# Kernel optimization log

Measured on AMD Instinct MI355X. Metric: run time of the kernel, lower is better.

The kernel has to match this reference:

```python
import jax, jax.numpy as jnp
import numpy as np

B, S, D, H = 2, 4096, 1024, 16
HD = D // H  # 64
BASE = 10000.0


def setup_inputs() -> dict:
    key = jax.random.key(0)
    ks = jax.random.split(key, 11)
    s = 1.0 / np.sqrt(D)
    return {
        "consulta": jax.random.normal(ks[0], (B, S, D), jnp.float32),
        "chave": jax.random.normal(ks[1], (B, S, D), jnp.float32),
        "valor": jax.random.normal(ks[2], (B, S, D), jnp.float32),
        "Wq": jax.random.normal(ks[3], (D, D), jnp.float32) * s,
        "bq": jnp.zeros((D,), jnp.float32),
        "Wk": jax.random.normal(ks[4], (D, D), jnp.float32) * s,
        "bk": jnp.zeros((D,), jnp.float32),
        "Wv": jax.random.normal(ks[5], (D, D), jnp.float32) * s,
        "bv": jnp.zeros((D,), jnp.float32),
        "Wo": jax.random.normal(ks[6], (D, D), jnp.float32) * s,
        "bo": jnp.zeros((D,), jnp.float32),
    }


def _rope(x):
    # x: [B, H, S, HD]; rotate interleaved (even, odd) pairs
    seq = x.shape[2]
    theta = 1.0 / (BASE ** (jnp.arange(0, HD, 2, dtype=jnp.float32) / HD))  # [HD/2]
    angles = jnp.arange(seq, dtype=jnp.float32)[:, None] * theta[None, :]  # [S, HD/2]
    cos, sin = jnp.cos(angles), jnp.sin(angles)
    xr = x.reshape(*x.shape[:-1], HD // 2, 2)
    x_re, x_im = xr[..., 0], xr[..., 1]
    out_re = x_re * cos - x_im * sin
    out_im = x_re * sin + x_im * cos
    return jnp.stack([out_re, out_im], axis=-1).reshape(x.shape)


def reference(consulta, chave, valor, Wq, bq, Wk, bk, Wv, bv, Wo, bo):
    b, s, _ = consulta.shape
    # projections (torch Linear: x @ W.T + b)
    Q = consulta @ Wq.T + bq
    K = chave @ Wk.T + bk
    V = valor @ Wv.T + bv
    # [B, H, S, HD]
    Q = Q.reshape(b, s, H, HD).transpose(0, 2, 1, 3)
    K = K.reshape(b, s, H, HD).transpose(0, 2, 1, 3)
    V = V.reshape(b, s, H, HD).transpose(0, 2, 1, 3)
    Q = _rope(Q)
    K = _rope(K)
    scores = jnp.einsum('bhqd,bhkd->bhqk', Q, K) / jnp.sqrt(jnp.float32(HD))
    weights = jax.nn.softmax(scores, axis=-1)  # dropout p=0 -> identity
    out = jnp.einsum('bhqk,bhkd->bhqd', weights, V)
    out = out.transpose(0, 2, 1, 3).reshape(b, s, D)
    return out @ Wo.T + bo
```

## Files before the change

### kernel.cpp

```cpp
#include <hip/hip_runtime.h>
#include <hip/hip_bf16.h>

typedef __attribute__((ext_vector_type(8))) short short8;
typedef __attribute__((ext_vector_type(4))) float f32x4;
typedef __attribute__((ext_vector_type(4))) unsigned short ushort4v;
typedef __attribute__((ext_vector_type(4))) float float4v;
typedef __attribute__((ext_vector_type(2))) unsigned int uint32x2;

#define NB 2
#define NS 4096
#define ND 1024
#define NH 16
#define NHD 64

#define QSCALE 0.18033688011112042f

__device__ __forceinline__ unsigned short f2bf(float x) {
    union { float f; unsigned u; } v; v.f = x;
    unsigned r = v.u + 0x7FFFu + ((v.u >> 16) & 1u);
    return (unsigned short)(r >> 16);
}

__device__ __forceinline__ unsigned cvt_pk_bf16(float lo, float hi) {
    unsigned r;
    asm("v_cvt_pk_bf16_f32 %0, %1, %2" : "=v"(r) : "v"(lo), "v"(hi));
    return r;
}

__device__ __forceinline__ void gload_lds16(const unsigned short* g, unsigned short* l) {
    __builtin_amdgcn_global_load_lds(
        (const __attribute__((address_space(1))) void*)g,
        (__attribute__((address_space(3))) void*)l,
        16, 0, 0);
}

__global__ void rope_table_kernel(float* __restrict__ cosT, float* __restrict__ sinT) {
    int i = blockIdx.x * blockDim.x + threadIdx.x;
    int p = i & 31, s = i >> 5;
    float theta = exp2f(-(float)(2 * p) * (13.287712379549449f / 64.0f));
    float ang = (float)s * theta;
    float sv, cv;
    sincosf(ang, &sv, &cv);
    cosT[i] = cv; sinT[i] = sv;
}

__global__ void cast_bf16_kernel(const float* __restrict__ in, unsigned short* __restrict__ out, int n8) {
    int i = blockIdx.x * blockDim.x + threadIdx.x;
    if (i >= n8) return;
    float4v a0 = *(const float4v*)(&in[(size_t)i * 8]);
    float4v a1 = *(const float4v*)(&in[(size_t)i * 8 + 4]);
    short8 s8;
    s8[0] = (short)f2bf(a0.x); s8[1] = (short)f2bf(a0.y);
    s8[2] = (short)f2bf(a0.z); s8[3] = (short)f2bf(a0.w);
    s8[4] = (short)f2bf(a1.x); s8[5] = (short)f2bf(a1.y);
    s8[6] = (short)f2bf(a1.z); s8[7] = (short)f2bf(a1.w);
    *(short8*)(&out[(size_t)i * 8]) = s8;
}

template<int EPI>
__global__ __launch_bounds__(256, 2) void gemm_kernel(
    const unsigned short* __restrict__ A,
    const unsigned short* __restrict__ Wb,
    const float* __restrict__ bias,
    void* __restrict__ outv,
    const float* __restrict__ cosT,
    const float* __restrict__ sinT,
    float oscale)
{
    __shared__ unsigned short As[128 * 32];
    __shared__ unsigned short Bs[128 * 32];
    const int t = threadIdx.x;
    const int wave = t >> 6, lane = t & 63;
    const int quad = lane >> 4, l15 = lane & 15;
    const int wm = (wave & 1) * 64, wn = (wave >> 1) * 64;
    const int m0 = blockIdx.y * 128, n0 = blockIdx.x * 128;

    f32x4 acc[4][4];
#pragma unroll
    for (int i = 0; i < 4; i++)
#pragma unroll
        for (int j = 0; j < 4; j++)
            acc[i][j] = f32x4{0.f, 0.f, 0.f, 0.f};

    for (int k0 = 0; k0 < ND; k0 += 32) {
#pragma unroll
        for (int p = 0; p < 2; p++) {
            int idx = p * 256 + t;
            int r = idx >> 2, c = (idx & 3) * 8;
            unsigned short* ldsA = &As[(size_t)(p * 256 + wave * 64) * 8];
            unsigned short* ldsB = &Bs[(size_t)(p * 256 + wave * 64) * 8];
            gload_lds16(&A[(size_t)(m0 + r) * ND + k0 + c], ldsA);
            gload_lds16(&Wb[(size_t)(n0 + r) * ND + k0 + c], ldsB);
        }
        __syncthreads();

        short8 af[4], bfr[4];
#pragma unroll
        for (int mt = 0; mt < 4; mt++)
            af[mt] = *(const short8*)(&As[(wm + mt * 16 + l15) * 32 + quad * 8]);
#pragma unroll
        for (int nt = 0; nt < 4; nt++)
            bfr[nt] = *(const short8*)(&Bs[(wn + nt * 16 + l15) * 32 + quad * 8]);
#pragma unroll
        for (int mt = 0; mt < 4; mt++)
#pragma unroll
            for (int nt = 0; nt < 4; nt++) {
                if (EPI == 0)
                    acc[mt][nt] = __builtin_amdgcn_mfma_f32_16x16x32_bf16(bfr[nt], af[mt], acc[mt][nt], 0, 0, 0);
                else
                    acc[mt][nt] = __builtin_amdgcn_mfma_f32_16x16x32_bf16(af[mt], bfr[nt], acc[mt][nt], 0, 0, 0);
            }
        __syncthreads();
    }

    if (EPI == 0) {
        float* out = (float*)outv;
#pragma unroll
        for (int mt = 0; mt < 4; mt++) {
            int gm = m0 + wm + mt * 16 + l15;
#pragma unroll
            for (int nt = 0; nt < 4; nt++) {
                int gn0 = n0 + wn + nt * 16 + quad * 4;
                float4v fv;
#pragma unroll
                for (int r = 0; r < 4; r++)
                    fv[r] = acc[mt][nt][r] + bias[gn0 + r];
                *(float4v*)(&out[(size_t)gm * ND + gn0]) = fv;
            }
        }
    } else if (EPI == 1) {
        unsigned short* out = (unsigned short*)outv;
#pragma unroll
        for (int nt = 0; nt < 4; nt++) {
            int gn = n0 + wn + nt * 16 + l15;
            int h = gn >> 6, hd = gn & 63, pr = hd >> 1, im = gn & 1;
            float bv = bias[gn];
#pragma unroll
            for (int mt = 0; mt < 4; mt++) {
                int gm0 = m0 + wm + mt * 16 + quad * 4;
#pragma unroll
                for (int r = 0; r < 4; r++) {
                    int gm = gm0 + r;
                    int b = gm >> 12, s = gm & 4095;
                    float v = acc[mt][nt][r] + bv;
                    float pv = __shfl_xor(v, 1, 64);
                    float cv = cosT[s * 32 + pr], sv = sinT[s * 32 + pr];
                    float o = im ? (pv * sv + v * cv) : (v * cv - pv * sv);
                    out[((size_t)(b * NH + h) * NS + s) * NHD + hd] = f2bf(o * oscale);
                }
            }
        }
    } else {
        unsigned short* out = (unsigned short*)outv;
#pragma unroll
        for (int nt = 0; nt < 4; nt++) {
            int gn = n0 + wn + nt * 16 + l15;
            int h = gn >> 6, hd = gn & 63;
            float bv = bias[gn];
#pragma unroll
            for (int mt = 0; mt < 4; mt++) {
                int gm0 = m0 + wm + mt * 16 + quad * 4;
                int b = gm0 >> 12, s0 = gm0 & 4095;
                ushort4v pk;
#pragma unroll
                for (int r = 0; r < 4; r++)
                    pk[r] = f2bf(acc[mt][nt][r] + bv);
                *(ushort4v*)(&out[((size_t)(b * NH + h) * NHD + hd) * NS + s0]) = pk;
            }
        }
    }
}

__global__ __launch_bounds__(256, 2) void flash_kernel(
    const unsigned short* __restrict__ Qr,
    const unsigned short* __restrict__ Kr,
    const unsigned short* __restrict__ Vt,
    unsigned short* __restrict__ Yatt)
{
    __shared__ unsigned short Ks[128 * 72];
    __shared__ unsigned short Vs[64 * 136];
    __shared__ unsigned short Pw[4][16 * 136];
    const int t = threadIdx.x;
    const int wave = t >> 6, lane = t & 63;
    const int quad = lane >> 4, l15 = lane & 15;
    const int bh = blockIdx.y;
    const int qb = blockIdx.x * 128;
    const int wq = wave * 32;
    const size_t base = (size_t)bh * NS * NHD;

    short8 qf[2][2];
#pragma unroll
    for (int nt = 0; nt < 2; nt++)
#pragma unroll
        for (int kk = 0; kk < 2; kk++)
            qf[nt][kk] = *(const short8*)(&Qr[base + (size_t)(qb + wq + nt * 16 + l15) * NHD + kk * 32 + quad * 8]);

    f32x4 accO[4][2];
#pragma unroll
    for (int i = 0; i < 4; i++)
#pragma unroll
        for (int j = 0; j < 2; j++)
            accO[i][j] = f32x4{0.f, 0.f, 0.f, 0.f};
    float mrow[2] = {-1e30f, -1e30f};
    float lrow[2] = {0.f, 0.f};

    for (int j0 = 0; j0 < NS; j0 += 128) {
#pragma unroll
        for (int p = 0; p < 4; p++) {
            int idx = p * 256 + t;
            { int r = idx >> 3, c = (idx & 7) * 8;
              *(short8*)(&Ks[r * 72 + c]) = *(const short8*)(&Kr[base + (size_t)(j0 + r) * NHD + c]); }
            { int r = idx >> 4, c = (idx & 15) * 8;
              *(short8*)(&Vs[r * 136 + c]) = *(const short8*)(&Vt[(size_t)(bh * NHD + r) * NS + j0 + c]); }
        }
        __syncthreads();

        f32x4 sa[8][2];
#pragma unroll
        for (int mt = 0; mt < 8; mt++)
#pragma unroll
            for (int nt = 0; nt < 2; nt++)
                sa[mt][nt] = f32x4{0.f, 0.f, 0.f, 0.f};
#pragma unroll
        for (int kk = 0; kk < 2; kk++)
#pragma unroll
            for (int mt = 0; mt < 8; mt++) {
                short8 ak = *(const short8*)(&Ks[(mt * 16 + l15) * 72 + kk * 32 + quad * 8]);
#pragma unroll
                for (int nt = 0; nt < 2; nt++)
                    sa[mt][nt] = __builtin_amdgcn_mfma_f32_16x16x32_bf16(ak, qf[nt][kk], sa[mt][nt], 0, 0, 0);
            }

#pragma unroll
        for (int nt = 0; nt < 2; nt++) {
            float mm[8];
#pragma unroll
            for (int mt = 0; mt < 8; mt++)
                mm[mt] = fmaxf(fmaxf(sa[mt][nt][0], sa[mt][nt][1]),
                               fmaxf(sa[mt][nt][2], sa[mt][nt][3]));
            float mx = fmaxf(fmaxf(fmaxf(mm[0], mm[1]), fmaxf(mm[2], mm[3])),
                             fmaxf(fmaxf(mm[4], mm[5]), fmaxf(mm[6], mm[7])));
            mx = fmaxf(mx, __shfl_xor(mx, 16, 64));
            mx = fmaxf(mx, __shfl_xor(mx, 32, 64));
            float mnew = fmaxf(mrow[nt], mx);
            float alpha = exp2f(mrow[nt] - mnew);
            float ls0 = 0.f, ls1 = 0.f, ls2 = 0.f, ls3 = 0.f;
#pragma unroll
            for (int mt = 0; mt < 8; mt++) {
                float p0 = exp2f(sa[mt][nt][0] - mnew);
                float p1 = exp2f(sa[mt][nt][1] - mnew);
                float p2 = exp2f(sa[mt][nt][2] - mnew);
                float p3 = exp2f(sa[mt][nt][3] - mnew);
                ls0 += p0; ls1 += p1; ls2 += p2; ls3 += p3;
                uint32x2 pk;
                pk.x = cvt_pk_bf16(p0, p1);
                pk.y = cvt_pk_bf16(p2, p3);
                *(uint32x2*)(&Pw[wave][l15 * 136 + mt * 16 + quad * 4]) = pk;
            }
            float lsum = (ls0 + ls1) + (ls2 + ls3);
            lsum += __shfl_xor(lsum, 16, 64);
            lsum += __shfl_xor(lsum, 32, 64);
            lrow[nt] = lrow[nt] * alpha + lsum;
            mrow[nt] = mnew;
#pragma unroll
            for (int mt2 = 0; mt2 < 4; mt2++)
#pragma unroll
                for (int r = 0; r < 4; r++)
                    accO[mt2][nt][r] *= alpha;

#pragma unroll
            for (int kk2 = 0; kk2 < 4; kk2++) {
                short8 av[4];
#pragma unroll
                for (int mt2 = 0; mt2 < 4; mt2++)
                    av[mt2] = *(const short8*)(&Vs[(mt2 * 16 + l15) * 136 + kk2 * 32 + quad * 8]);
                short8 bp = *(const short8*)(&Pw[wave][l15 * 136 + kk2 * 32 + quad * 8]);
#pragma unroll
                for (int mt2 = 0; mt2 < 4; mt2++)
                    accO[mt2][nt] = __builtin_amdgcn_mfma_f32_16x16x32_bf16(av[mt2], bp, accO[mt2][nt], 0, 0, 0);
            }
        }
        __syncthreads();
    }

    int b = bh >> 4, h = bh & 15;
#pragma unroll
    for (int nt = 0; nt < 2; nt++) {
        float rl = 1.f / lrow[nt];
        int s = qb + wq + nt * 16 + l15;
#pragma unroll
        for (int mt2 = 0; mt2 < 4; mt2++) {
            uint32x2 pk;
            pk.x = cvt_pk_bf16(accO[mt2][nt][0] * rl, accO[mt2][nt][1] * rl);
            pk.y = cvt_pk_bf16(accO[mt2][nt][2] * rl, accO[mt2][nt][3] * rl);
            *(uint32x2*)(&Yatt[((size_t)(b * NS + s)) * ND + h * NHD + mt2 * 16 + quad * 4]) = pk;
        }
    }
}

extern "C" void kernel_launch(void* const* d_in, const int* in_sizes, int n_in,
                              void* d_out, int out_size, void* d_ws, size_t ws_size,
                              hipStream_t stream) {
    const float* consulta = (const float*)d_in[0];
    const float* chave    = (const float*)d_in[1];
    const float* valor    = (const float*)d_in[2];
    const float* Wq = (const float*)d_in[3];
    const float* bq = (const float*)d_in[4];
    const float* Wk = (const float*)d_in[5];
    const float* bk = (const float*)d_in[6];
    const float* Wv = (const float*)d_in[7];
    const float* bv = (const float*)d_in[8];
    const float* Wo = (const float*)d_in[9];
    const float* bo = (const float*)d_in[10];

    const size_t NX = (size_t)8192 * 1024;

    float* cosT = (float*)d_ws;
    float* sinT = cosT + (size_t)NS * 32;
    unsigned short* Qrb = (unsigned short*)(sinT + (size_t)NS * 32);
    unsigned short* Krb = Qrb + NX;
    unsigned short* Vtb = Krb + NX;
    unsigned short* Yat = Vtb + NX;
    unsigned short* Abf = Yat + NX;
    unsigned short* Wbf = Abf + NX;

    rope_table_kernel<<<NS * 32 / 256, 256, 0, stream>>>(cosT, sinT);

    const int ACT8 = (int)(NX / 8);
    const int W8 = ND * ND / 8;

    dim3 ggrid(8, 64);

    cast_bf16_kernel<<<ACT8 / 256, 256, 0, stream>>>(consulta, Abf, ACT8);
    cast_bf16_kernel<<<W8 / 256, 256, 0, stream>>>(Wq, Wbf, W8);
    gemm_kernel<1><<<ggrid, 256, 0, stream>>>(Abf, Wbf, bq, Qrb, cosT, sinT, QSCALE);

    cast_bf16_kernel<<<ACT8 / 256, 256, 0, stream>>>(chave, Abf, ACT8);
    cast_bf16_kernel<<<W8 / 256, 256, 0, stream>>>(Wk, Wbf, W8);
    gemm_kernel<1><<<ggrid, 256, 0, stream>>>(Abf, Wbf, bk, Krb, cosT, sinT, 1.0f);

    cast_bf16_kernel<<<ACT8 / 256, 256, 0, stream>>>(valor, Abf, ACT8);
    cast_bf16_kernel<<<W8 / 256, 256, 0, stream>>>(Wv, Wbf, W8);
    gemm_kernel<2><<<ggrid, 256, 0, stream>>>(Abf, Wbf, bv, Vtb, cosT, sinT, 1.0f);

    flash_kernel<<<dim3(32, 32), 256, 0, stream>>>(Qrb, Krb, Vtb, Yat);

    cast_bf16_kernel<<<W8 / 256, 256, 0, stream>>>(Wo, Wbf, W8);
    gemm_kernel<0><<<ggrid, 256, 0, stream>>>(Yat, Wbf, bo, d_out, cosT, sinT, 1.0f);
}
```

Before: 587.6 us.

## Prefetch next K/V tile into registers and batch PV MFMAs with lazy rescale

Loads the next K/V tile from global memory into registers before the current tile's compute, then writes it to shared memory after a barrier, so global latency overlaps the MFMA work. The P tile now stores both 16-row groups, which lets the PV MFMAs for both row groups be interleaved in one loop. The online-softmax rescale is skipped while the running max grows by at most 8 (log2 units). s_setprio is raised around the MFMA blocks. The cost is more registers from the prefetch buffers and more LDS for Pw, which may reduce occupancy under launch_bounds(256,2).

```diff
diff --git a/kernel.cpp b/kernel.cpp
--- a/kernel.cpp
+++ b/kernel.cpp
@@ -179,7 +179,7 @@
 {
     __shared__ unsigned short Ks[128 * 72];
     __shared__ unsigned short Vs[64 * 136];
-    __shared__ unsigned short Pw[4][16 * 136];
+    __shared__ unsigned short Pw[4][32 * 136];
     const int t = threadIdx.x;
     const int wave = t >> 6, lane = t & 63;
     const int quad = lane >> 4, l15 = lane & 15;
@@ -204,16 +204,35 @@
     float mrow[2] = {-1e30f, -1e30f};
     float lrow[2] = {0.f, 0.f};
 
+#pragma unroll
+    for (int p = 0; p < 4; p++) {
+        int idx = p * 256 + t;
+        { int r = idx >> 3, c = (idx & 7) * 8;
+          *(short8*)(&Ks[r * 72 + c]) = *(const short8*)(&Kr[base + (size_t)r * NHD + c]); }
+        { int r = idx >> 4, c = (idx & 15) * 8;
+          *(short8*)(&Vs[r * 136 + c]) = *(const short8*)(&Vt[(size_t)(bh * NHD + r) * NS + c]); }
+    }
+    __syncthreads();
+
     for (int j0 = 0; j0 < NS; j0 += 128) {
-#pragma unroll
-        for (int p = 0; p < 4; p++) {
-            int idx = p * 256 + t;
-            { int r = idx >> 3, c = (idx & 7) * 8;
-              *(short8*)(&Ks[r * 72 + c]) = *(const short8*)(&Kr[base + (size_t)(j0 + r) * NHD + c]); }
-            { int r = idx >> 4, c = (idx & 15) * 8;
-              *(short8*)(&Vs[r * 136 + c]) = *(const short8*)(&Vt[(size_t)(bh * NHD + r) * NS + j0 + c]); }
-        }
-        __syncthreads();
+        const bool more = (j0 + 128) < NS;
+
+        short8 kpr0, kpr1, kpr2, kpr3, vpr0, vpr1, vpr2, vpr3;
+        if (more) {
+            int j1 = j0 + 128;
+#pragma unroll
+            for (int p = 0; p < 4; p++) {
+                int idx = p * 256 + t;
+                int rk = idx >> 3, ck = (idx & 7) * 8;
+                int rv = idx >> 4, cv = (idx & 15) * 8;
+                short8 kv = *(const short8*)(&Kr[base + (size_t)(j1 + rk) * NHD + ck]);
+                short8 vv = *(const short8*)(&Vt[(size_t)(bh * NHD + rv) * NS + j1 + cv]);
+                if (p == 0) { kpr0 = kv; vpr0 = vv; }
+                else if (p == 1) { kpr1 = kv; vpr1 = vv; }
+                else if (p == 2) { kpr2 = kv; vpr2 = vv; }
+                else { kpr3 = kv; vpr3 = vv; }
+            }
+        }
 
         f32x4 sa[8][2];
 #pragma unroll
@@ -221,6 +240,7 @@
 #pragma unroll
             for (int nt = 0; nt < 2; nt++)
                 sa[mt][nt] = f32x4{0.f, 0.f, 0.f, 0.f};
+        __builtin_amdgcn_s_setprio(1);
 #pragma unroll
         for (int kk = 0; kk < 2; kk++)
 #pragma unroll
@@ -230,6 +250,7 @@
                 for (int nt = 0; nt < 2; nt++)
                     sa[mt][nt] = __builtin_amdgcn_mfma_f32_16x16x32_bf16(ak, qf[nt][kk], sa[mt][nt], 0, 0, 0);
             }
+        __builtin_amdgcn_s_setprio(0);
 
 #pragma unroll
         for (int nt = 0; nt < 2; nt++) {
@@ -242,42 +263,66 @@
                              fmaxf(fmaxf(mm[4], mm[5]), fmaxf(mm[6], mm[7])));
             mx = fmaxf(mx, __shfl_xor(mx, 16, 64));
             mx = fmaxf(mx, __shfl_xor(mx, 32, 64));
-            float mnew = fmaxf(mrow[nt], mx);
-            float alpha = exp2f(mrow[nt] - mnew);
+            if (!__all(mx <= mrow[nt] + 8.0f)) {
+                float mnew = fmaxf(mrow[nt], mx);
+                float alpha = exp2f(mrow[nt] - mnew);
+                lrow[nt] *= alpha;
+#pragma unroll
+                for (int mt2 = 0; mt2 < 4; mt2++)
+#pragma unroll
+                    for (int r = 0; r < 4; r++)
+                        accO[mt2][nt][r] *= alpha;
+                mrow[nt] = mnew;
+            }
+            float mcur = mrow[nt];
             float ls0 = 0.f, ls1 = 0.f, ls2 = 0.f, ls3 = 0.f;
 #pragma unroll
             for (int mt = 0; mt < 8; mt++) {
-                float p0 = exp2f(sa[mt][nt][0] - mnew);
-                float p1 = exp2f(sa[mt][nt][1] - mnew);
-                float p2 = exp2f(sa[mt][nt][2] - mnew);
-                float p3 = exp2f(sa[mt][nt][3] - mnew);
+                float p0 = exp2f(sa[mt][nt][0] - mcur);
+                float p1 = exp2f(sa[mt][nt][1] - mcur);
+                float p2 = exp2f(sa[mt][nt][2] - mcur);
+                float p3 = exp2f(sa[mt][nt][3] - mcur);
                 ls0 += p0; ls1 += p1; ls2 += p2; ls3 += p3;
                 uint32x2 pk;
                 pk.x = cvt_pk_bf16(p0, p1);
                 pk.y = cvt_pk_bf16(p2, p3);
-                *(uint32x2*)(&Pw[wave][l15 * 136 + mt * 16 + quad * 4]) = pk;
+                *(uint32x2*)(&Pw[wave][(nt * 16 + l15) * 136 + mt * 16 + quad * 4]) = pk;
             }
             float lsum = (ls0 + ls1) + (ls2 + ls3);
             lsum += __shfl_xor(lsum, 16, 64);
             lsum += __shfl_xor(lsum, 32, 64);
-            lrow[nt] = lrow[nt] * alpha + lsum;
-            mrow[nt] = mnew;
+            lrow[nt] += lsum;
+        }
+
+        __builtin_amdgcn_s_setprio(1);
+#pragma unroll
+        for (int kk2 = 0; kk2 < 4; kk2++) {
+            short8 av[4], bp[2];
 #pragma unroll
             for (int mt2 = 0; mt2 < 4; mt2++)
-#pragma unroll
-                for (int r = 0; r < 4; r++)
-                    accO[mt2][nt][r] *= alpha;
-
-#pragma unroll
-            for (int kk2 = 0; kk2 < 4; kk2++) {
-                short8 av[4];
-#pragma unroll
-                for (int mt2 = 0; mt2 < 4; mt2++)
-                    av[mt2] = *(const short8*)(&Vs[(mt2 * 16 + l15) * 136 + kk2 * 32 + quad * 8]);
-                short8 bp = *(const short8*)(&Pw[wave][l15 * 136 + kk2 * 32 + quad * 8]);
-#pragma unroll
-                for (int mt2 = 0; mt2 < 4; mt2++)
-                    accO[mt2][nt] = __builtin_amdgcn_mfma_f32_16x16x32_bf16(av[mt2], bp, accO[mt2][nt], 0, 0, 0);
+                av[mt2] = *(const short8*)(&Vs[(mt2 * 16 + l15) * 136 + kk2 * 32 + quad * 8]);
+#pragma unroll
+            for (int nt = 0; nt < 2; nt++)
+                bp[nt] = *(const short8*)(&Pw[wave][(nt * 16 + l15) * 136 + kk2 * 32 + quad * 8]);
+#pragma unroll
+            for (int mt2 = 0; mt2 < 4; mt2++)
+#pragma unroll
+                for (int nt = 0; nt < 2; nt++)
+                    accO[mt2][nt] = __builtin_amdgcn_mfma_f32_16x16x32_bf16(av[mt2], bp[nt], accO[mt2][nt], 0, 0, 0);
+        }
+        __builtin_amdgcn_s_setprio(0);
+
+        __syncthreads();
+        if (more) {
+#pragma unroll
+            for (int p = 0; p < 4; p++) {
+                int idx = p * 256 + t;
+                int rk = idx >> 3, ck = (idx & 7) * 8;
+                int rv = idx >> 4, cv = (idx & 15) * 8;
+                short8 kv = (p == 0) ? kpr0 : (p == 1) ? kpr1 : (p == 2) ? kpr2 : kpr3;
+                short8 vv = (p == 0) ? vpr0 : (p == 1) ? vpr1 : (p == 2) ? vpr2 : vpr3;
+                *(short8*)(&Ks[rk * 72 + ck]) = kv;
+                *(short8*)(&Vs[rv * 136 + cv]) = vv;
             }
         }
         __syncthreads();
```

Result: faster. 560.1 us (-4.7%).

## Rewrite flash attention inner loop with 32x32 MFMA and register-resident P

Applied to the files above, without the earlier changes.

Switches the flash kernel from 16x16x32 to 32x32x16 bf16 MFMA tiles so each wave owns 32 query rows with one running max and sum per lane. The softmax probabilities stay in registers and are rearranged with v_permlane32_swap instead of going through a per-wave LDS buffer, which removes LDS traffic and the shared P array. It also skips the accumulator rescale unless the row max grows by more than 8 (lazy rescaling), and raises wave priority around the MFMA blocks. The larger 16-float accumulators increase register pressure, which may hurt occupancy under launch_bounds(256,2).

```diff
diff --git a/kernel.cpp b/kernel.cpp
--- a/kernel.cpp
+++ b/kernel.cpp
@@ -3,9 +3,11 @@
 
 typedef __attribute__((ext_vector_type(8))) short short8;
 typedef __attribute__((ext_vector_type(4))) float f32x4;
+typedef __attribute__((ext_vector_type(16))) float f32x16;
 typedef __attribute__((ext_vector_type(4))) unsigned short ushort4v;
 typedef __attribute__((ext_vector_type(4))) float float4v;
 typedef __attribute__((ext_vector_type(2))) unsigned int uint32x2;
+typedef __attribute__((ext_vector_type(4))) unsigned int uint32x4;
 
 #define NB 2
 #define NS 4096
@@ -179,30 +181,26 @@
 {
     __shared__ unsigned short Ks[128 * 72];
     __shared__ unsigned short Vs[64 * 136];
-    __shared__ unsigned short Pw[4][16 * 136];
     const int t = threadIdx.x;
     const int wave = t >> 6, lane = t & 63;
-    const int quad = lane >> 4, l15 = lane & 15;
+    const int l31 = lane & 31, h = lane >> 5;
     const int bh = blockIdx.y;
     const int qb = blockIdx.x * 128;
     const int wq = wave * 32;
     const size_t base = (size_t)bh * NS * NHD;
 
-    short8 qf[2][2];
-#pragma unroll
-    for (int nt = 0; nt < 2; nt++)
-#pragma unroll
-        for (int kk = 0; kk < 2; kk++)
-            qf[nt][kk] = *(const short8*)(&Qr[base + (size_t)(qb + wq + nt * 16 + l15) * NHD + kk * 32 + quad * 8]);
-
-    f32x4 accO[4][2];
-#pragma unroll
-    for (int i = 0; i < 4; i++)
-#pragma unroll
-        for (int j = 0; j < 2; j++)
-            accO[i][j] = f32x4{0.f, 0.f, 0.f, 0.f};
-    float mrow[2] = {-1e30f, -1e30f};
-    float lrow[2] = {0.f, 0.f};
+    short8 qf[4];
+#pragma unroll
+    for (int ks = 0; ks < 4; ks++)
+        qf[ks] = *(const short8*)(&Qr[base + (size_t)(qb + wq + l31) * NHD + ks * 16 + h * 8]);
+
+    f32x16 accO[2];
+#pragma unroll
+    for (int dt = 0; dt < 2; dt++)
+#pragma unroll
+        for (int r = 0; r < 16; r++)
+            accO[dt][r] = 0.f;
+    float mrow = -1e30f, lrow = 0.f;
 
     for (int j0 = 0; j0 < NS; j0 += 128) {
 #pragma unroll
@@ -215,87 +213,101 @@
         }
         __syncthreads();
 
-        f32x4 sa[8][2];
-#pragma unroll
-        for (int mt = 0; mt < 8; mt++)
-#pragma unroll
-            for (int nt = 0; nt < 2; nt++)
-                sa[mt][nt] = f32x4{0.f, 0.f, 0.f, 0.f};
-#pragma unroll
-        for (int kk = 0; kk < 2; kk++)
-#pragma unroll
-            for (int mt = 0; mt < 8; mt++) {
-                short8 ak = *(const short8*)(&Ks[(mt * 16 + l15) * 72 + kk * 32 + quad * 8]);
-#pragma unroll
-                for (int nt = 0; nt < 2; nt++)
-                    sa[mt][nt] = __builtin_amdgcn_mfma_f32_16x16x32_bf16(ak, qf[nt][kk], sa[mt][nt], 0, 0, 0);
-            }
-
-#pragma unroll
-        for (int nt = 0; nt < 2; nt++) {
-            float mm[8];
-#pragma unroll
-            for (int mt = 0; mt < 8; mt++)
-                mm[mt] = fmaxf(fmaxf(sa[mt][nt][0], sa[mt][nt][1]),
-                               fmaxf(sa[mt][nt][2], sa[mt][nt][3]));
-            float mx = fmaxf(fmaxf(fmaxf(mm[0], mm[1]), fmaxf(mm[2], mm[3])),
-                             fmaxf(fmaxf(mm[4], mm[5]), fmaxf(mm[6], mm[7])));
-            mx = fmaxf(mx, __shfl_xor(mx, 16, 64));
-            mx = fmaxf(mx, __shfl_xor(mx, 32, 64));
-            float mnew = fmaxf(mrow[nt], mx);
-            float alpha = exp2f(mrow[nt] - mnew);
-            float ls0 = 0.f, ls1 = 0.f, ls2 = 0.f, ls3 = 0.f;
-#pragma unroll
-            for (int mt = 0; mt < 8; mt++) {
-                float p0 = exp2f(sa[mt][nt][0] - mnew);
-                float p1 = exp2f(sa[mt][nt][1] - mnew);
-                float p2 = exp2f(sa[mt][nt][2] - mnew);
-                float p3 = exp2f(sa[mt][nt][3] - mnew);
+        f32x16 sa[4];
+#pragma unroll
+        for (int kt = 0; kt < 4; kt++)
+#pragma unroll
+            for (int r = 0; r < 16; r++)
+                sa[kt][r] = 0.f;
+        __builtin_amdgcn_s_setprio(1);
+#pragma unroll
+        for (int kt = 0; kt < 4; kt++)
+#pragma unroll
+            for (int ks = 0; ks < 4; ks++) {
+                short8 ak = *(const short8*)(&Ks[(kt * 32 + l31) * 72 + ks * 16 + h * 8]);
+                sa[kt] = __builtin_amdgcn_mfma_f32_32x32x16_bf16(ak, qf[ks], sa[kt], 0, 0, 0);
+            }
+        __builtin_amdgcn_s_setprio(0);
+
+        float mx = -1e30f;
+#pragma unroll
+        for (int kt = 0; kt < 4; kt++) {
+            float m0v = fmaxf(fmaxf(sa[kt][0], sa[kt][1]), fmaxf(sa[kt][2], sa[kt][3]));
+            float m1v = fmaxf(fmaxf(sa[kt][4], sa[kt][5]), fmaxf(sa[kt][6], sa[kt][7]));
+            float m2v = fmaxf(fmaxf(sa[kt][8], sa[kt][9]), fmaxf(sa[kt][10], sa[kt][11]));
+            float m3v = fmaxf(fmaxf(sa[kt][12], sa[kt][13]), fmaxf(sa[kt][14], sa[kt][15]));
+            mx = fmaxf(mx, fmaxf(fmaxf(m0v, m1v), fmaxf(m2v, m3v)));
+        }
+        mx = fmaxf(mx, __shfl_xor(mx, 32, 64));
+        if (!__all(mx <= mrow + 8.0f)) {
+            float mnew = fmaxf(mrow, mx);
+            float alpha = exp2f(mrow - mnew);
+            lrow *= alpha;
+#pragma unroll
+            for (int dt = 0; dt < 2; dt++)
+#pragma unroll
+                for (int r = 0; r < 16; r++)
+                    accO[dt][r] *= alpha;
+            mrow = mnew;
+        }
+        float ls0 = 0.f, ls1 = 0.f, ls2 = 0.f, ls3 = 0.f;
+        unsigned pk[4][4][2];
+#pragma unroll
+        for (int kt = 0; kt < 4; kt++)
+#pragma unroll
+            for (int g = 0; g < 4; g++) {
+                float p0 = exp2f(sa[kt][4 * g + 0] - mrow);
+                float p1 = exp2f(sa[kt][4 * g + 1] - mrow);
+                float p2 = exp2f(sa[kt][4 * g + 2] - mrow);
+                float p3 = exp2f(sa[kt][4 * g + 3] - mrow);
                 ls0 += p0; ls1 += p1; ls2 += p2; ls3 += p3;
-                uint32x2 pk;
-                pk.x = cvt_pk_bf16(p0, p1);
-                pk.y = cvt_pk_bf16(p2, p3);
-                *(uint32x2*)(&Pw[wave][l15 * 136 + mt * 16 + quad * 4]) = pk;
-            }
-            float lsum = (ls0 + ls1) + (ls2 + ls3);
-            lsum += __shfl_xor(lsum, 16, 64);
-            lsum += __shfl_xor(lsum, 32, 64);
-            lrow[nt] = lrow[nt] * alpha + lsum;
-            mrow[nt] = mnew;
-#pragma unroll
-            for (int mt2 = 0; mt2 < 4; mt2++)
-#pragma unroll
-                for (int r = 0; r < 4; r++)
-                    accO[mt2][nt][r] *= alpha;
-
-#pragma unroll
-            for (int kk2 = 0; kk2 < 4; kk2++) {
-                short8 av[4];
-#pragma unroll
-                for (int mt2 = 0; mt2 < 4; mt2++)
-                    av[mt2] = *(const short8*)(&Vs[(mt2 * 16 + l15) * 136 + kk2 * 32 + quad * 8]);
-                short8 bp = *(const short8*)(&Pw[wave][l15 * 136 + kk2 * 32 + quad * 8]);
-#pragma unroll
-                for (int mt2 = 0; mt2 < 4; mt2++)
-                    accO[mt2][nt] = __builtin_amdgcn_mfma_f32_16x16x32_bf16(av[mt2], bp, accO[mt2][nt], 0, 0, 0);
-            }
-        }
+                pk[kt][g][0] = cvt_pk_bf16(p0, p1);
+                pk[kt][g][1] = cvt_pk_bf16(p2, p3);
+            }
+        float lsum = (ls0 + ls1) + (ls2 + ls3);
+        lsum += __shfl_xor(lsum, 32, 64);
+        lrow += lsum;
+
+#pragma unroll
+        for (int t2 = 0; t2 < 4; t2++)
+#pragma unroll
+            for (int u = 0; u < 2; u++)
+#pragma unroll
+                for (int j = 0; j < 2; j++)
+                    asm volatile("v_permlane32_swap_b32 %0, %1"
+                                 : "+v"(pk[t2][2 * u][j]), "+v"(pk[t2][2 * u + 1][j]));
+
+        __builtin_amdgcn_s_setprio(1);
+#pragma unroll
+        for (int ks2 = 0; ks2 < 8; ks2++) {
+            const int t2 = ks2 >> 1, u = ks2 & 1;
+            uint32x4 bw;
+            bw.x = pk[t2][2 * u][0];     bw.y = pk[t2][2 * u][1];
+            bw.z = pk[t2][2 * u + 1][0]; bw.w = pk[t2][2 * u + 1][1];
+            short8 bp = __builtin_bit_cast(short8, bw);
+#pragma unroll
+            for (int dt = 0; dt < 2; dt++) {
+                short8 av = *(const short8*)(&Vs[(dt * 32 + l31) * 136 + ks2 * 16 + h * 8]);
+                accO[dt] = __builtin_amdgcn_mfma_f32_32x32x16_bf16(av, bp, accO[dt], 0, 0, 0);
+            }
+        }
+        __builtin_amdgcn_s_setprio(0);
         __syncthreads();
     }
 
-    int b = bh >> 4, h = bh & 15;
-#pragma unroll
-    for (int nt = 0; nt < 2; nt++) {
-        float rl = 1.f / lrow[nt];
-        int s = qb + wq + nt * 16 + l15;
-#pragma unroll
-        for (int mt2 = 0; mt2 < 4; mt2++) {
-            uint32x2 pk;
-            pk.x = cvt_pk_bf16(accO[mt2][nt][0] * rl, accO[mt2][nt][1] * rl);
-            pk.y = cvt_pk_bf16(accO[mt2][nt][2] * rl, accO[mt2][nt][3] * rl);
-            *(uint32x2*)(&Yatt[((size_t)(b * NS + s)) * ND + h * NHD + mt2 * 16 + quad * 4]) = pk;
-        }
-    }
+    int b = bh >> 4, hh = bh & 15;
+    float rl = 1.f / lrow;
+    int s = qb + wq + l31;
+#pragma unroll
+    for (int dt = 0; dt < 2; dt++)
+#pragma unroll
+        for (int g = 0; g < 4; g++) {
+            uint32x2 w;
+            w.x = cvt_pk_bf16(accO[dt][4 * g + 0] * rl, accO[dt][4 * g + 1] * rl);
+            w.y = cvt_pk_bf16(accO[dt][4 * g + 2] * rl, accO[dt][4 * g + 3] * rl);
+            int d0 = dt * 32 + 8 * g + 4 * h;
+            *(uint32x2*)(&Yatt[((size_t)(b * NS + s)) * ND + hh * NHD + d0]) = w;
+        }
 }
 
 extern "C" void kernel_launch(void* const* d_in, const int* in_sizes, int n_in,
```

New measurement: 518.4 us. 1.13x faster.
